# Performance work log

Hardware: AMD Instinct MI355X
Metric: run time of the kernel (lower is better)

The kernel has to match this reference:

```python
import jax, jax.numpy as jnp
import numpy as np

B, S, E, H, V = 64, 400, 512, 512, 32000


def setup_inputs() -> dict:
    key = jax.random.key(0)
    ks = jax.random.split(key, 16)
    sc = lambda fan: 1.0 / np.sqrt(fan)
    u = lambda k, shape, fan: jax.random.uniform(k, shape, jnp.float32, -sc(fan), sc(fan))
    mask = jax.random.randint(ks[3], (B, S), 0, 2).astype(bool)
    mask = mask.at[:, 0].set(True)  # ensure at least one valid position per row
    return {
        "decoder_input": jax.random.normal(ks[0], (B, E), jnp.float32),
        "previous_hidden_state": jax.random.normal(ks[1], (B, H), jnp.float32),
        "encoder_output": jax.random.normal(ks[2], (B, S, 2 * H), jnp.float32),
        "mask": mask,
        # GRUCell params (torch layout: weight_ih [3H,E], weight_hh [3H,H])
        "w_ih": u(ks[4], (3 * H, E), H),
        "w_hh": u(ks[5], (3 * H, H), H),
        "b_ih": u(ks[6], (3 * H,), H),
        "b_hh": u(ks[7], (3 * H,), H),
        # Attention params
        "Wh_w": u(ks[8], (H, 2 * H), 2 * H),
        "Wh_b": u(ks[9], (H,), 2 * H),
        "Ws_w": u(ks[10], (H, H), H),
        "Ws_b": u(ks[11], (H,), H),
        "vatt_w": u(ks[12], (1, H), H),  # Linear(H,1,bias=False)
        # Output projections
        "V_w": u(ks[13], (H, 3 * H), 3 * H),
        "V_b": u(ks[13], (H,), 3 * H),
        "Vhat_w": u(ks[14], (V, H), H),
        "Vhat_b": u(ks[15], (V,), H),
    }


def reference(decoder_input, previous_hidden_state, encoder_output, mask,
              w_ih, w_hh, b_ih, b_hh, Wh_w, Wh_b, Ws_w, Ws_b, vatt_w,
              V_w, V_b, Vhat_w, Vhat_b):
    # --- GRUCell step (torch semantics) ---
    gi = decoder_input @ w_ih.T + b_ih                  # [B, 3H]
    gh = previous_hidden_state @ w_hh.T + b_hh          # [B, 3H]
    i_r, i_z, i_n = jnp.split(gi, 3, axis=-1)
    h_r, h_z, h_n = jnp.split(gh, 3, axis=-1)
    r = jax.nn.sigmoid(i_r + h_r)
    z = jax.nn.sigmoid(i_z + h_z)
    n = jnp.tanh(i_n + r * h_n)
    hidden = (1.0 - z) * n + z * previous_hidden_state  # [B, H]

    # --- Additive (Bahdanau) attention ---
    feat = jnp.tanh(encoder_output @ Wh_w.T + Wh_b
                    + (hidden @ Ws_w.T + Ws_b)[:, None, :])   # [B, S, H]
    scores = jnp.einsum('bsh,h->bs', feat, vatt_w[0])          # [B, S]
    scores = jnp.where(mask, scores, -jnp.inf)
    attn_dist = jax.nn.softmax(scores, axis=-1)                # [B, S]

    # --- Context + output projection ---
    context_vector = jnp.einsum('bs,bsd->bd', attn_dist, encoder_output)  # [B, 2H]
    out = jnp.concatenate([hidden, context_vector], axis=-1) @ V_w.T + V_b  # [B, H]
    logits = out @ Vhat_w.T + Vhat_b                                        # [B, V]
    vocab_dist = jax.nn.softmax(logits, axis=-1)
    return (vocab_dist, attn_dist, context_vector, hidden)
```

## Files before the change

### kernel.cpp

```cpp
#include <hip/hip_runtime.h>
#include <hip/hip_bf16.h>
#include <stdint.h>

#define DI __device__ __forceinline__

using f32x2 = __attribute__((ext_vector_type(2))) float;
using f32x4 = __attribute__((ext_vector_type(4))) float;
using s16x8 = __attribute__((ext_vector_type(8))) short;

#define BB 64
#define SS 400
#define HH 512
#define VVOC 32000
#define MTOT (BB*SS)

DI short bf16r(float f){
  __hip_bfloat16 h = __float2bfloat16(f);
  union { __hip_bfloat16 h; short s; } u; u.h = h; return u.s;
}
DI float sigm(float x){ return 1.f/(1.f + __expf(-x)); }
DI float tanhfast(float x){ x = fminf(x, 12.f); float e = __expf(2.f*x); return (e-1.f)/(e+1.f); }

DI void gload16b(const __hip_bfloat16* g, short* l){
  __builtin_amdgcn_global_load_lds(
      (const __attribute__((address_space(1))) __hip_bfloat16*)g,
      (__attribute__((address_space(3))) short*)l, 16, 0, 0);
}

DI float blkmax(float v, float* red, int t){
  #pragma unroll
  for (int o = 32; o; o >>= 1) v = fmaxf(v, __shfl_xor(v, o));
  if ((t & 63) == 0) red[t >> 6] = v;
  __syncthreads();
  v = fmaxf(fmaxf(red[0], red[1]), fmaxf(red[2], red[3]));
  __syncthreads();
  return v;
}
DI float blksum(float v, float* red, int t){
  #pragma unroll
  for (int o = 32; o; o >>= 1) v += __shfl_xor(v, o);
  if ((t & 63) == 0) red[t >> 6] = v;
  __syncthreads();
  v = red[0] + red[1] + red[2] + red[3];
  __syncthreads();
  return v;
}

DI s16x8 cvt8v(f32x4 a, f32x4 b){
  s16x8 o;
  o[0]=bf16r(a[0]); o[1]=bf16r(a[1]); o[2]=bf16r(a[2]); o[3]=bf16r(a[3]);
  o[4]=bf16r(b[0]); o[5]=bf16r(b[1]); o[6]=bf16r(b[2]); o[7]=bf16r(b[3]);
  return o;
}
DI s16x8 cvt8(const float* src){
  return cvt8v(((const f32x4*)src)[0], ((const f32x4*)src)[1]);
}

DI s16x8 fragload16(const short* tile, int rbase, int kk, int l){
  int r = rbase + (l & 15);
  int c = (kk >> 3) + (l >> 4);
  int slot = c ^ (r & 7);
  return *(const s16x8*)(tile + r*64 + slot*8);
}

DI void mfma_small_body(const float* __restrict__ A, const float* __restrict__ W,
                        float* __restrict__ P, int K, int N, int c0, int kseg,
                        short* lsa, short* lsb, int t)
{
  const int kbeg = kseg*64;
  const int l = t & 63, w = t >> 6;
  #pragma unroll
  for (int q = 0; q < 2; ++q) {
    int it = q*256 + t;
    int r = it >> 3, c = it & 7;
    int slot = (c ^ (r & 7)) << 3;
    *(s16x8*)(lsa + r*64 + slot) = cvt8(A + (size_t)r*K + kbeg + c*8);
    *(s16x8*)(lsb + r*64 + slot) = cvt8(W + (size_t)(c0 + r)*K + kbeg + c*8);
  }
  __syncthreads();
  f32x4 acc[4];
  #pragma unroll
  for (int m = 0; m < 4; ++m) { f32x4 z = {0.f,0.f,0.f,0.f}; acc[m] = z; }
  #pragma unroll
  for (int kk = 0; kk < 64; kk += 32) {
    s16x8 bf = fragload16(lsb, w*16, kk, l);
    #pragma unroll
    for (int m = 0; m < 4; ++m) {
      s16x8 af = fragload16(lsa, m*16, kk, l);
      acc[m] = __builtin_amdgcn_mfma_f32_16x16x32_bf16(af, bf, acc[m], 0, 0, 0);
    }
  }
  const int kq = l >> 4, lc = l & 15;
  const int col = c0 + w*16 + lc;
  size_t pbase = (size_t)kseg * 64 * N;
  #pragma unroll
  for (int m = 0; m < 4; ++m)
    #pragma unroll
    for (int j = 0; j < 4; ++j)
      P[pbase + (size_t)(m*16 + kq*4 + j)*N + col] = acc[m][j];
}

__global__ __launch_bounds__(256) void k_pre(
    const float* __restrict__ wh, short* __restrict__ wh16,
    const unsigned int* __restrict__ mask, int mwords, int* __restrict__ flags,
    const float* __restrict__ x, const float* __restrict__ hprev,
    const float* __restrict__ w_ih, const float* __restrict__ w_hh,
    float* __restrict__ GI, float* __restrict__ GH)
{
  __shared__ __align__(16) short ls[2][64*64];
  int b = blockIdx.x, t = threadIdx.x;
  if (b < 256) {
    int i = b*256 + t;
    ((s16x8*)wh16)[i] = cvt8(wh + (size_t)i*8);
  } else if (b < 264) {
    __shared__ int f;
    if (t == 0) f = 0;
    __syncthreads();
    int loc = 0;
    for (int i = (b-256)*256 + t; i < mwords; i += 8*256) loc |= (mask[i] > 1u) ? 1 : 0;
    if (loc) atomicOr(&f, 1);
    __syncthreads();
    if (t == 0) flags[b-256] = f;
  } else {
    int gb = b - 264;
    int colI = gb % 24;
    int kseg = (gb / 24) % 8;
    int z    = gb / 192;
    mfma_small_body(z ? hprev : x, z ? w_hh : w_ih, z ? GH : GI,
                    512, 1536, colI*64, kseg, ls[0], ls[1], t);
  }
}

__global__ void gru_gate(const float* __restrict__ GI, const float* __restrict__ GH,
                         const float* __restrict__ b_ih, const float* __restrict__ b_hh,
                         const float* __restrict__ hprev, float* __restrict__ hid,
                         float* __restrict__ concat)
{
  int i = blockIdx.x*256 + threadIdx.x;
  int b = i >> 9, h = i & 511;
  float ir=0, iz=0, inn=0, hr=0, hz=0, hn=0;
  #pragma unroll
  for (int s = 0; s < 8; ++s) {
    const float* gi = GI + (size_t)s*(64*1536) + b*1536;
    const float* gh = GH + (size_t)s*(64*1536) + b*1536;
    ir += gi[h];      iz += gi[512+h];  inn += gi[1024+h];
    hr += gh[h];      hz += gh[512+h];  hn  += gh[1024+h];
  }
  ir += b_ih[h]; iz += b_ih[512+h]; inn += b_ih[1024+h];
  hr += b_hh[h]; hz += b_hh[512+h]; hn  += b_hh[1024+h];
  float r = sigm(ir + hr), z = sigm(iz + hz);
  float n = tanhfast(inn + r*hn);
  float hv = (1.f - z)*n + z*hprev[i];
  hid[i] = hv;
  concat[b*1536 + h] = hv;
}

__global__ __launch_bounds__(256) void mfma_small(
    const float* __restrict__ A, const float* __restrict__ W,
    float* __restrict__ P, int K, int N)
{
  __shared__ __align__(16) short ls[2][64*64];
  mfma_small_body(A, W, P, K, N, blockIdx.x*64, blockIdx.y, ls[0], ls[1], threadIdx.x);
}

__global__ void combineN(const float* __restrict__ P, const float* __restrict__ b1,
                         const float* __restrict__ b2, float* __restrict__ dstv,
                         int N, int total, int nseg)
{
  int i = blockIdx.x*256 + threadIdx.x;
  if (i >= total) return;
  float a = 0.f;
  for (int s = 0; s < nseg; ++s) a += P[(size_t)s*total + i];
  int c = i % N;
  if (b1) a += b1[c];
  if (b2) a += b2[c];
  dstv[i] = a;
}

__global__ __launch_bounds__(256) void score_gemm_bf16(
    const float* __restrict__ A, const __hip_bfloat16* __restrict__ Bw,
    const float* __restrict__ qv, const float* __restrict__ vb, float* __restrict__ dst)
{
  __shared__ __align__(16) short lsa[2][64*64];
  __shared__ __align__(16) short lsb[2][128*64];
  const int t = threadIdx.x;
  const int l = t & 63;
  const int w = t >> 6;
  const int wm = w >> 1;
  const int wn = w & 1;
  const int phys = blockIdx.x;
  const int logical = (phys & 7)*200 + (phys >> 3);
  const int mrow = (logical >> 2) * 64;
  const int colb = logical & 3;
  const int ncol = colb * 128;

  const int ar = t >> 2;
  const int aq = t & 3;
  const float* abase = A + (size_t)(mrow + ar)*1024 + aq*16;
  const int as0 = ((2*aq    ) ^ (ar & 7)) << 3;
  const int as1 = ((2*aq + 1) ^ (ar & 7)) << 3;

  f32x4 acc[2][4];
  #pragma unroll
  for (int m = 0; m < 2; ++m)
    #pragma unroll
    for (int n = 0; n < 4; ++n) { f32x4 z = {0.f,0.f,0.f,0.f}; acc[m][n] = z; }

  f32x4 pa0, pa1, pa2, pa3;
  #define A_LOAD(k0) { const f32x4* ap = (const f32x4*)(abase + (k0));            \
                       pa0 = ap[0]; pa1 = ap[1]; pa2 = ap[2]; pa3 = ap[3]; }
  #define A_WRITE(buf) { *(s16x8*)(&lsa[buf][ar*64] + as0) = cvt8v(pa0, pa1);     \
                         *(s16x8*)(&lsa[buf][ar*64] + as1) = cvt8v(pa2, pa3); }
  #define B_STAGE(buf, k0)                                                        \
    _Pragma("unroll")                                                              \
    for (int i = 0; i < 4; ++i) {                                                  \
      int ci = i*256 + t;                                                          \
      int r = ci >> 3, slot = ci & 7;                                              \
      int c = slot ^ (r & 7);                                                      \
      gload16b(Bw + (size_t)(ncol + r)*1024 + (k0) + c*8, &lsb[buf][ci*8]);        \
    }

  A_LOAD(0)
  B_STAGE(0, 0)
  A_WRITE(0)
  __syncthreads();

  int cur = 0;
  for (int k = 0; k < 16; ++k) {
    if (k < 15) {
      A_LOAD((k+1)*64)
      B_STAGE(cur ^ 1, (k+1)*64)
    }
    #pragma unroll
    for (int kk = 0; kk < 64; kk += 32) {
      s16x8 bf[4];
      #pragma unroll
      for (int n = 0; n < 4; ++n) bf[n] = fragload16(lsb[cur], wn*64 + n*16, kk, l);
      #pragma unroll
      for (int m = 0; m < 2; ++m) {
        s16x8 af = fragload16(lsa[cur], wm*32 + m*16, kk, l);
        #pragma unroll
        for (int n = 0; n < 4; ++n)
          acc[m][n] = __builtin_amdgcn_mfma_f32_16x16x32_bf16(af, bf[n], acc[m][n], 0, 0, 0);
      }
    }
    if (k < 15) A_WRITE(cur ^ 1)
    __syncthreads();
    cur ^= 1;
  }
  #undef A_LOAD
  #undef A_WRITE
  #undef B_STAGE

  const int kq = l >> 4, lc = l & 15;
  float vv[4];
  #pragma unroll
  for (int n = 0; n < 4; ++n) vv[n] = vb[ncol + wn*64 + n*16 + lc];
  const int seg = colb*2 + wn;
  #pragma unroll
  for (int m = 0; m < 2; ++m) {
    #pragma unroll
    for (int j = 0; j < 4; ++j) {
      int r = mrow + wm*32 + m*16 + kq*4 + j;
      int b = r / SS;
      const float* qb = qv + b*HH + ncol + wn*64 + lc;
      float ps = 0.f;
      #pragma unroll
      for (int n = 0; n < 4; ++n) ps += vv[n]*tanhfast(acc[m][n][j] + qb[n*16]);
      #pragma unroll
      for (int o = 1; o < 16; o <<= 1) ps += __shfl_xor(ps, o);
      if (lc == 0) dst[seg*MTOT + r] = ps;
    }
  }
}

__global__ __launch_bounds__(256) void vocab_gemm(
    const float* __restrict__ OUTm, const float* __restrict__ Vhat,
    const float* __restrict__ Vb, float* __restrict__ logits,
    float* __restrict__ MAXP, float* __restrict__ SUMP)
{
  __shared__ __align__(16) short lsa[64*64];
  __shared__ __align__(16) short lsb[64*64];
  __shared__ float red[64][8];
  const int t = threadIdx.x, l = t & 63, w = t >> 6;
  const int vrow0 = blockIdx.x * 64;

  f32x4 acc[4];
  #pragma unroll
  for (int m = 0; m < 4; ++m) { f32x4 z = {0.f,0.f,0.f,0.f}; acc[m] = z; }

  f32x4 pa0[2][2], pb0[2][2], pa1[2][2], pb1[2][2];

  #define VLOAD(pa, pb, k0)                                                     \
    _Pragma("unroll")                                                           \
    for (int q = 0; q < 2; ++q) {                                               \
      int it = q*256 + t; int r = it >> 3, c = it & 7;                          \
      const f32x4* ap = (const f32x4*)(OUTm + (size_t)r*512 + (k0) + c*8);      \
      pa[q][0] = ap[0]; pa[q][1] = ap[1];                                       \
      const f32x4* bp = (const f32x4*)(Vhat + (size_t)(vrow0 + r)*512 + (k0) + c*8); \
      pb[q][0] = bp[0]; pb[q][1] = bp[1];                                       \
    }
  #define VSTEP(pa, pb)                                                         \
    _Pragma("unroll")                                                           \
    for (int q = 0; q < 2; ++q) {                                               \
      int it = q*256 + t; int r = it >> 3, c = it & 7;                          \
      int slot = (c ^ (r & 7)) << 3;                                            \
      *(s16x8*)(lsa + r*64 + slot) = cvt8v(pa[q][0], pa[q][1]);                 \
      *(s16x8*)(lsb + r*64 + slot) = cvt8v(pb[q][0], pb[q][1]);                 \
    }                                                                           \
    __syncthreads();                                                            \
    _Pragma("unroll")                                                           \
    for (int kk = 0; kk < 64; kk += 32) {                                       \
      s16x8 bf = fragload16(lsb, w*16, kk, l);                                  \
      _Pragma("unroll")                                                         \
      for (int m = 0; m < 4; ++m) {                                             \
        s16x8 af = fragload16(lsa, m*16, kk, l);                                \
        acc[m] = __builtin_amdgcn_mfma_f32_16x16x32_bf16(af, bf, acc[m], 0,0,0);\
      }                                                                         \
    }                                                                           \
    __syncthreads();

  VLOAD(pa0, pb0, 0)
  #pragma unroll
  for (int s2 = 0; s2 < 4; ++s2) {
    int k0 = s2*128;
    if (k0 + 64 < 512) { VLOAD(pa1, pb1, k0 + 64) }
    VSTEP(pa0, pb0)
    if (k0 + 128 < 512) { VLOAD(pa0, pb0, k0 + 128) }
    VSTEP(pa1, pb1)
  }
  #undef VLOAD
  #undef VSTEP

  const int kq = l >> 4, lc = l & 15;
  const int voc = vrow0 + w*16 + lc;
  const float bias = Vb[voc];
  #pragma unroll
  for (int m = 0; m < 4; ++m)
    #pragma unroll
    for (int j = 0; j < 4; ++j) {
      acc[m][j] += bias;
      logits[(size_t)(m*16 + kq*4 + j)*VVOC + voc] = acc[m][j];
    }
  #pragma unroll
  for (int m = 0; m < 4; ++m)
    #pragma unroll
    for (int j = 0; j < 4; ++j) {
      float v = acc[m][j];
      #pragma unroll
      for (int o = 1; o < 16; o <<= 1) v = fmaxf(v, __shfl_xor(v, o));
      if (lc == 0) red[m*16 + kq*4 + j][w] = v;
    }
  __syncthreads();
  float gmax[4][4];
  #pragma unroll
  for (int m = 0; m < 4; ++m)
    #pragma unroll
    for (int j = 0; j < 4; ++j) {
      int row = m*16 + kq*4 + j;
      gmax[m][j] = fmaxf(fmaxf(red[row][0], red[row][1]), fmaxf(red[row][2], red[row][3]));
    }
  __syncthreads();
  #pragma unroll
  for (int m = 0; m < 4; ++m)
    #pragma unroll
    for (int j = 0; j < 4; ++j) {
      float s = __expf(acc[m][j] - gmax[m][j]);
      #pragma unroll
      for (int o = 1; o < 16; o <<= 1) s += __shfl_xor(s, o);
      if (lc == 0) red[m*16 + kq*4 + j][4 + w] = s;
    }
  __syncthreads();
  if (t < 64) {
    float M = fmaxf(fmaxf(red[t][0], red[t][1]), fmaxf(red[t][2], red[t][3]));
    float S = red[t][4] + red[t][5] + red[t][6] + red[t][7];
    MAXP[blockIdx.x*64 + t] = M;
    SUMP[blockIdx.x*64 + t] = S;
  }
}

__global__ __launch_bounds__(256) void vnorm(
    const float* __restrict__ MAXP, const float* __restrict__ SUMP,
    float* __restrict__ logits)
{
  __shared__ float red[4];
  int b = blockIdx.x, q = blockIdx.y, t = threadIdx.x;
  float m = -INFINITY;
  for (int i = t; i < 500; i += 256) m = fmaxf(m, MAXP[i*64 + b]);
  m = blkmax(m, red, t);
  float z = 0.f;
  for (int i = t; i < 500; i += 256) z += SUMP[i*64 + b] * __expf(MAXP[i*64 + b] - m);
  z = blksum(z, red, t);
  float inv = 1.f / z;
  f32x4* p = (f32x4*)(logits + (size_t)b*VVOC + q*8000);
  for (int i = t; i < 2000; i += 256) {
    f32x4 v = p[i];
    #pragma unroll
    for (int c = 0; c < 4; ++c) v[c] = __expf(v[c] - m) * inv;
    p[i] = v;
  }
}

__global__ void softmax_s(const float* __restrict__ part, const void* __restrict__ mask,
                          const int* __restrict__ flags, float* __restrict__ attn)
{
  __shared__ float red[4];
  int b = blockIdx.x, t = threadIdx.x;
  bool isbyte = (flags[0]|flags[1]|flags[2]|flags[3]|flags[4]|flags[5]|flags[6]|flags[7]) != 0;
  float sc0, sc1 = -INFINITY;
  {
    float v = 0.f;
    #pragma unroll
    for (int p = 0; p < 8; ++p) v += part[p*MTOT + b*SS + t];
    bool mv = isbyte ? (((const unsigned char*)mask)[b*SS + t] != 0)
                     : (((const int*)mask)[b*SS + t] != 0);
    sc0 = mv ? v : -INFINITY;
  }
  int s1 = t + 256;
  if (s1 < SS) {
    float v = 0.f;
    #pragma unroll
    for (int p = 0; p < 8; ++p) v += part[p*MTOT + b*SS + s1];
    bool mv = isbyte ? (((const unsigned char*)mask)[b*SS + s1] != 0)
                     : (((const int*)mask)[b*SS + s1] != 0);
    sc1 = mv ? v : -INFINITY;
  }
  float mx = blkmax(fmaxf(sc0, sc1), red, t);
  float e0 = __expf(sc0 - mx), e1 = __expf(sc1 - mx);
  float sum = blksum(e0 + e1, red, t);
  float inv = 1.f / sum;
  attn[b*SS + t] = e0 * inv;
  if (s1 < SS) attn[b*SS + s1] = e1 * inv;
}

__global__ void ctx_part(const float* __restrict__ attn, const float* __restrict__ enc,
                         float* __restrict__ CTXP)
{
  int b = blockIdx.x, dh = blockIdx.y, sq = blockIdx.z;
  int d0 = dh*512 + threadIdx.x*2;
  const float* a = attn + b*SS + sq*50;
  const float* e = enc + (size_t)(b*SS + sq*50)*1024 + d0;
  float lo = 0.f, hi = 0.f;
  #pragma unroll 5
  for (int s = 0; s < 50; ++s) {
    f32x2 u = *(const f32x2*)(e + (size_t)s*1024);
    float av = a[s];
    lo += av * u[0];
    hi += av * u[1];
  }
  float* dst = CTXP + (size_t)sq*65536 + b*1024 + d0;
  dst[0] = lo; dst[1] = hi;
}

__global__ void ctx_combine(const float* __restrict__ CTXP, float* __restrict__ ctx,
                            float* __restrict__ concat)
{
  int b = blockIdx.x;
  for (int d = threadIdx.x; d < 1024; d += 256) {
    float s = 0.f;
    #pragma unroll
    for (int q = 0; q < 8; ++q) s += CTXP[q*65536 + b*1024 + d];
    ctx[b*1024 + d] = s;
    concat[b*1536 + 512 + d] = s;
  }
}

extern "C" void kernel_launch(void* const* d_in, const int* in_sizes, int n_in,
                              void* d_out, int out_size, void* d_ws, size_t ws_size,
                              hipStream_t stream) {
  (void)in_sizes; (void)n_in; (void)out_size; (void)ws_size;
  const float* x      = (const float*)d_in[0];
  const float* hprev  = (const float*)d_in[1];
  const float* enc    = (const float*)d_in[2];
  const void*  mask   = d_in[3];
  const float* w_ih   = (const float*)d_in[4];
  const float* w_hh   = (const float*)d_in[5];
  const float* b_ih   = (const float*)d_in[6];
  const float* b_hh   = (const float*)d_in[7];
  const float* Wh_w   = (const float*)d_in[8];
  const float* Wh_b   = (const float*)d_in[9];
  const float* Ws_w   = (const float*)d_in[10];
  const float* Ws_b   = (const float*)d_in[11];
  const float* vatt   = (const float*)d_in[12];
  const float* V_w    = (const float*)d_in[13];
  const float* V_b    = (const float*)d_in[14];
  const float* Vhat_w = (const float*)d_in[15];
  const float* Vhat_b = (const float*)d_in[16];

  float* out   = (float*)d_out;
  float* vocab = out;
  float* attn  = out + 2048000;
  float* ctx   = out + 2073600;
  float* hid   = out + 2139136;

  float* WS     = (float*)d_ws;
  int*   FLAGS  = (int*)d_ws;
  float* GI     = WS + 16;
  float* GH     = GI + 786432;
  float* QP     = GH + 786432;
  float* Q      = QP + 262144;
  float* OUT    = Q + 32768;
  float* PART   = OUT + 32768;
  float* MAXP   = PART + 204800;
  float* SUMP   = MAXP + 32000;
  float* CTXP   = SUMP + 32000;
  float* OUTP   = CTXP + 524288;
  float* CONCAT = OUTP + 786432;
  float* ENDF   = CONCAT + 98304;
  size_t f32_bytes = ((size_t)((char*)ENDF - (char*)d_ws) + 15) & ~(size_t)15;
  short* WH16  = (short*)((char*)d_ws + f32_bytes);

  k_pre<<<dim3(648), 256, 0, stream>>>(Wh_w, WH16, (const unsigned int*)mask, 6400, FLAGS,
                                       x, hprev, w_ih, w_hh, GI, GH);
  gru_gate<<<dim3(128), 256, 0, stream>>>(GI, GH, b_ih, b_hh, hprev, hid, CONCAT);
  mfma_small<<<dim3(8, 8), 256, 0, stream>>>(hid, Ws_w, QP, 512, 512);
  combineN<<<dim3(128), 256, 0, stream>>>(QP, Ws_b, Wh_b, Q, 512, 32768, 8);
  score_gemm_bf16<<<dim3(1600), 256, 0, stream>>>(
      enc, (const __hip_bfloat16*)WH16, Q, vatt, PART);
  softmax_s<<<dim3(64), 256, 0, stream>>>(PART, mask, FLAGS, attn);
  ctx_part<<<dim3(64, 2, 8), 256, 0, stream>>>(attn, enc, CTXP);
  ctx_combine<<<dim3(64), 256, 0, stream>>>(CTXP, ctx, CONCAT);
  mfma_small<<<dim3(8, 24), 256, 0, stream>>>(CONCAT, V_w, OUTP, 1536, 512);
  combineN<<<dim3(128), 256, 0, stream>>>(OUTP, V_b, nullptr, OUT, 512, 32768, 24);
  vocab_gemm<<<dim3(500), 256, 0, stream>>>(OUT, Vhat_w, Vhat_b, vocab, MAXP, SUMP);
  vnorm<<<dim3(64, 4), 256, 0, stream>>>(MAXP, SUMP, vocab);
}
```

Before: 152.6 us.

## Widen score GEMM tile to full H, reducing partial scores in-block

Each score GEMM block now covers 128 encoder rows and all 512 hidden columns with 512 threads, so every encoder row is read and converted to bf16 once instead of four times. The per-column-tile partial scores are summed in shared memory, and the block writes a single score per row, which removes the 8-way partial buffer and the summation in the softmax kernel. The cost is the loss of double buffering (one LDS buffer with two barriers per k-step), a much larger accumulator footprint (128 floats per thread) that limits occupancy, and only 200 blocks to spread across the CUs.

```diff
diff --git a/kernel.cpp b/kernel.cpp
--- a/kernel.cpp
+++ b/kernel.cpp
@@ -177,100 +177,102 @@
   dstv[i] = a;
 }
 
-__global__ __launch_bounds__(256) void score_gemm_bf16(
+__global__ __launch_bounds__(512) void score_gemm_bf16(
     const float* __restrict__ A, const __hip_bfloat16* __restrict__ Bw,
     const float* __restrict__ qv, const float* __restrict__ vb, float* __restrict__ dst)
 {
-  __shared__ __align__(16) short lsa[2][64*64];
-  __shared__ __align__(16) short lsb[2][128*64];
+  __shared__ __align__(16) short lsa[128*64];
+  __shared__ __align__(16) short lsb[512*64];
   const int t = threadIdx.x;
   const int l = t & 63;
   const int w = t >> 6;
-  const int wm = w >> 1;
-  const int wn = w & 1;
+  const int wm = w >> 2;
+  const int wn = w & 3;
   const int phys = blockIdx.x;
-  const int logical = (phys & 7)*200 + (phys >> 3);
-  const int mrow = (logical >> 2) * 64;
-  const int colb = logical & 3;
-  const int ncol = colb * 128;
-
-  const int ar = t >> 2;
-  const int aq = t & 3;
-  const float* abase = A + (size_t)(mrow + ar)*1024 + aq*16;
-  const int as0 = ((2*aq    ) ^ (ar & 7)) << 3;
-  const int as1 = ((2*aq + 1) ^ (ar & 7)) << 3;
-
-  f32x4 acc[2][4];
-  #pragma unroll
-  for (int m = 0; m < 2; ++m)
-    #pragma unroll
-    for (int n = 0; n < 4; ++n) { f32x4 z = {0.f,0.f,0.f,0.f}; acc[m][n] = z; }
-
-  f32x4 pa0, pa1, pa2, pa3;
-  #define A_LOAD(k0) { const f32x4* ap = (const f32x4*)(abase + (k0));            \
-                       pa0 = ap[0]; pa1 = ap[1]; pa2 = ap[2]; pa3 = ap[3]; }
-  #define A_WRITE(buf) { *(s16x8*)(&lsa[buf][ar*64] + as0) = cvt8v(pa0, pa1);     \
-                         *(s16x8*)(&lsa[buf][ar*64] + as1) = cvt8v(pa2, pa3); }
-  #define B_STAGE(buf, k0)                                                        \
-    _Pragma("unroll")                                                              \
-    for (int i = 0; i < 4; ++i) {                                                  \
-      int ci = i*256 + t;                                                          \
-      int r = ci >> 3, slot = ci & 7;                                              \
-      int c = slot ^ (r & 7);                                                      \
-      gload16b(Bw + (size_t)(ncol + r)*1024 + (k0) + c*8, &lsb[buf][ci*8]);        \
-    }
+  const int logical = (phys & 7)*25 + (phys >> 3);
+  const int mrow = logical * 128;
+
+  f32x4 par[2][2];
+  #define A_LOAD(k0)                                                              \
+    _Pragma("unroll")                                                             \
+    for (int q = 0; q < 2; ++q) {                                                 \
+      int ci = q*512 + t; int r = ci >> 3, c = ci & 7;                            \
+      const f32x4* ap = (const f32x4*)(A + (size_t)(mrow + r)*1024 + (k0) + c*8); \
+      par[q][0] = ap[0]; par[q][1] = ap[1];                                       \
+    }
+  #define A_WRITE()                                                               \
+    _Pragma("unroll")                                                             \
+    for (int q = 0; q < 2; ++q) {                                                 \
+      int ci = q*512 + t; int r = ci >> 3, c = ci & 7;                            \
+      *(s16x8*)(lsa + r*64 + ((c ^ (r & 7)) << 3)) = cvt8v(par[q][0], par[q][1]); \
+    }
+  #define B_STAGE(k0)                                                             \
+    _Pragma("unroll")                                                             \
+    for (int i = 0; i < 8; ++i) {                                                 \
+      int ci = i*512 + t; int r = ci >> 3, slot = ci & 7;                         \
+      int c = slot ^ (r & 7);                                                     \
+      gload16b(Bw + (size_t)r*1024 + (k0) + c*8, lsb + ci*8);                     \
+    }
+
+  f32x4 acc[4][8];
+  #pragma unroll
+  for (int m = 0; m < 4; ++m)
+    #pragma unroll
+    for (int n = 0; n < 8; ++n) { f32x4 z = {0.f,0.f,0.f,0.f}; acc[m][n] = z; }
 
   A_LOAD(0)
-  B_STAGE(0, 0)
-  A_WRITE(0)
-  __syncthreads();
-
-  int cur = 0;
+  A_WRITE()
+  B_STAGE(0)
+  __syncthreads();
+
   for (int k = 0; k < 16; ++k) {
-    if (k < 15) {
-      A_LOAD((k+1)*64)
-      B_STAGE(cur ^ 1, (k+1)*64)
-    }
+    if (k < 15) A_LOAD((k+1)*64)
     #pragma unroll
     for (int kk = 0; kk < 64; kk += 32) {
-      s16x8 bf[4];
+      s16x8 bf[8];
       #pragma unroll
-      for (int n = 0; n < 4; ++n) bf[n] = fragload16(lsb[cur], wn*64 + n*16, kk, l);
+      for (int n = 0; n < 8; ++n) bf[n] = fragload16(lsb, wn*128 + n*16, kk, l);
       #pragma unroll
-      for (int m = 0; m < 2; ++m) {
-        s16x8 af = fragload16(lsa[cur], wm*32 + m*16, kk, l);
+      for (int m = 0; m < 4; ++m) {
+        s16x8 af = fragload16(lsa, wm*64 + m*16, kk, l);
         #pragma unroll
-        for (int n = 0; n < 4; ++n)
+        for (int n = 0; n < 8; ++n)
           acc[m][n] = __builtin_amdgcn_mfma_f32_16x16x32_bf16(af, bf[n], acc[m][n], 0, 0, 0);
       }
     }
-    if (k < 15) A_WRITE(cur ^ 1)
     __syncthreads();
-    cur ^= 1;
+    if (k < 15) { A_WRITE() B_STAGE((k+1)*64) }
+    __syncthreads();
   }
   #undef A_LOAD
   #undef A_WRITE
   #undef B_STAGE
 
   const int kq = l >> 4, lc = l & 15;
-  float vv[4];
-  #pragma unroll
-  for (int n = 0; n < 4; ++n) vv[n] = vb[ncol + wn*64 + n*16 + lc];
-  const int seg = colb*2 + wn;
-  #pragma unroll
-  for (int m = 0; m < 2; ++m) {
+  float vv[8];
+  #pragma unroll
+  for (int n = 0; n < 8; ++n) vv[n] = vb[wn*128 + n*16 + lc];
+  float* red = (float*)lsa;
+  #pragma unroll
+  for (int m = 0; m < 4; ++m) {
     #pragma unroll
     for (int j = 0; j < 4; ++j) {
-      int r = mrow + wm*32 + m*16 + kq*4 + j;
+      int rl = wm*64 + m*16 + kq*4 + j;
+      int r = mrow + rl;
       int b = r / SS;
-      const float* qb = qv + b*HH + ncol + wn*64 + lc;
+      const float* qb = qv + b*HH + wn*128 + lc;
       float ps = 0.f;
       #pragma unroll
-      for (int n = 0; n < 4; ++n) ps += vv[n]*tanhfast(acc[m][n][j] + qb[n*16]);
+      for (int n = 0; n < 8; ++n) ps += vv[n]*tanhfast(acc[m][n][j] + qb[n*16]);
       #pragma unroll
       for (int o = 1; o < 16; o <<= 1) ps += __shfl_xor(ps, o);
-      if (lc == 0) dst[seg*MTOT + r] = ps;
-    }
+      if (lc == 0) red[rl*4 + wn] = ps;
+    }
+  }
+  __syncthreads();
+  if (t < 128) {
+    float s = red[t*4] + red[t*4+1] + red[t*4+2] + red[t*4+3];
+    dst[mrow + t] = s;
   }
 }
 
@@ -401,7 +403,7 @@
   }
 }
 
-__global__ void softmax_s(const float* __restrict__ part, const void* __restrict__ mask,
+__global__ void softmax_s(const float* __restrict__ score, const void* __restrict__ mask,
                           const int* __restrict__ flags, float* __restrict__ attn)
 {
   __shared__ float red[4];
@@ -409,21 +411,15 @@
   bool isbyte = (flags[0]|flags[1]|flags[2]|flags[3]|flags[4]|flags[5]|flags[6]|flags[7]) != 0;
   float sc0, sc1 = -INFINITY;
   {
-    float v = 0.f;
-    #pragma unroll
-    for (int p = 0; p < 8; ++p) v += part[p*MTOT + b*SS + t];
     bool mv = isbyte ? (((const unsigned char*)mask)[b*SS + t] != 0)
                      : (((const int*)mask)[b*SS + t] != 0);
-    sc0 = mv ? v : -INFINITY;
+    sc0 = mv ? score[b*SS + t] : -INFINITY;
   }
   int s1 = t + 256;
   if (s1 < SS) {
-    float v = 0.f;
-    #pragma unroll
-    for (int p = 0; p < 8; ++p) v += part[p*MTOT + b*SS + s1];
     bool mv = isbyte ? (((const unsigned char*)mask)[b*SS + s1] != 0)
                      : (((const int*)mask)[b*SS + s1] != 0);
-    sc1 = mv ? v : -INFINITY;
+    sc1 = mv ? score[b*SS + s1] : -INFINITY;
   }
   float mx = blkmax(fmaxf(sc0, sc1), red, t);
   float e0 = __expf(sc0 - mx), e1 = __expf(sc1 - mx);
@@ -500,8 +496,8 @@
   float* QP     = GH + 786432;
   float* Q      = QP + 262144;
   float* OUT    = Q + 32768;
-  float* PART   = OUT + 32768;
-  float* MAXP   = PART + 204800;
+  float* SCORE  = OUT + 32768;
+  float* MAXP   = SCORE + 25600;
   float* SUMP   = MAXP + 32000;
   float* CTXP   = SUMP + 32000;
   float* OUTP   = CTXP + 524288;
@@ -515,9 +511,9 @@
   gru_gate<<<dim3(128), 256, 0, stream>>>(GI, GH, b_ih, b_hh, hprev, hid, CONCAT);
   mfma_small<<<dim3(8, 8), 256, 0, stream>>>(hid, Ws_w, QP, 512, 512);
   combineN<<<dim3(128), 256, 0, stream>>>(QP, Ws_b, Wh_b, Q, 512, 32768, 8);
-  score_gemm_bf16<<<dim3(1600), 256, 0, stream>>>(
-      enc, (const __hip_bfloat16*)WH16, Q, vatt, PART);
-  softmax_s<<<dim3(64), 256, 0, stream>>>(PART, mask, FLAGS, attn);
+  score_gemm_bf16<<<dim3(200), 512, 0, stream>>>(
+      enc, (const __hip_bfloat16*)WH16, Q, vatt, SCORE);
+  softmax_s<<<dim3(64), 256, 0, stream>>>(SCORE, mask, FLAGS, attn);
   ctx_part<<<dim3(64, 2, 8), 256, 0, stream>>>(attn, enc, CTXP);
   ctx_combine<<<dim3(64), 256, 0, stream>>>(CTXP, ctx, CONCAT);
   mfma_small<<<dim3(8, 24), 256, 0, stream>>>(CONCAT, V_w, OUTP, 1536, 512);
```

Result: faster. 134.2 us (-12.1%).
